# Kernel optimization log

Measured on AMD Instinct MI355X. Metric: run time of the kernel, lower is better.

The kernel has to match this reference:

```python
import jax, jax.numpy as jnp
import numpy as np

D = 1024
KERNEL = 4

def setup_inputs() -> dict:
    key = jax.random.key(0)
    ks = jax.random.split(key, 8)
    B, L, d = 4, 8192, D
    x = jax.random.normal(ks[0], (B, L, d), dtype=jnp.float32)
    conv_weight = jax.random.normal(ks[1], (d, 1, KERNEL), dtype=jnp.float32) * 0.02
    conv_bias = jnp.zeros((d,), dtype=jnp.float32)
    lim = 1.0 / np.sqrt(d)
    Wr_w = jax.random.uniform(ks[2], (d, d), jnp.float32, -lim, lim)
    Wr_b = jax.random.uniform(ks[3], (d,), jnp.float32, -lim, lim)
    Wi_w = jax.random.uniform(ks[4], (d, d), jnp.float32, -lim, lim)
    Wi_b = jax.random.uniform(ks[5], (d,), jnp.float32, -lim, lim)
    log_a = jnp.full((d,), 7.5, dtype=jnp.float32)
    out_w = jax.random.uniform(ks[6], (d, d), jnp.float32, -lim, lim)
    norm_w = jnp.ones((d,), dtype=jnp.float32)
    return {"x": x, "conv_weight": conv_weight, "conv_bias": conv_bias,
            "Wr_w": Wr_w, "Wr_b": Wr_b, "Wi_w": Wi_w, "Wi_b": Wi_b,
            "log_a": log_a, "out_w": out_w, "norm_w": norm_w}

def _causal_depthwise_conv(x, w, b):
    # x: [B,L,d], w: [d,1,K], b: [d]. out[t] = sum_k w[:,0,k] * x[t-3+k] + b
    B, L, d = x.shape
    xp = jnp.pad(x, ((0, 0), (KERNEL - 1, 0), (0, 0)))
    out = b[None, None, :]
    for k in range(KERNEL):  # small fixed kernel loop
        out = out + xp[:, k:k + L, :] * w[:, 0, k][None, None, :]
    return out

def _parallel_scan(a_t, b_t):
    # h_t = a_t * h_{t-1} + b_t via log-space cumsum; float32 throughout
    a = a_t.astype(jnp.float32)
    b = b_t.astype(jnp.float32)
    log_A = jnp.clip(jnp.cumsum(jnp.log(jnp.clip(a, 1e-7)), axis=1), -80.0, None)
    A = jnp.exp(log_A)
    h = A * jnp.cumsum(b * jnp.exp(-log_A), axis=1)
    return h.astype(a_t.dtype)

def _rmsnorm(x, w, eps=1e-6):
    ms = jnp.mean(jnp.square(x.astype(jnp.float32)), axis=-1, keepdims=True)
    return (x * jax.lax.rsqrt(ms + eps)).astype(x.dtype) * w

def reference(x, conv_weight, conv_bias, Wr_w, Wr_b, Wi_w, Wi_b, log_a, out_w, norm_w):
    x_conv = _causal_depthwise_conv(x, conv_weight, conv_bias)          # [B,L,d]
    r_t = jax.nn.sigmoid(x_conv @ Wr_w.T + Wr_b)
    i_t = jax.nn.sigmoid(x_conv @ Wi_w.T + Wi_b)
    a_base = jax.nn.sigmoid(log_a.astype(jnp.float32)).astype(x.dtype)
    a_t = jnp.power(a_base[None, None, :], 8.0 * r_t)
    b_t = jnp.sqrt(jnp.clip(1.0 - a_t * a_t, 1e-6, None)) * (i_t * x_conv)
    h = _parallel_scan(a_t, b_t)
    return _rmsnorm(h @ out_w.T, norm_w)
```

## Files before the change

kernel.cpp:

```cpp
#include <hip/hip_runtime.h>
#include <hip/hip_bf16.h>

#define D 1024
#define KW 4
#define SEQL 8192
#define BATCH 4
#define MROWS (BATCH*SEQL)
#define SEG 128
#define NSEG (SEQL/SEG)

using bf16 = __hip_bfloat16;
typedef __attribute__((ext_vector_type(8))) short bf16x8_t;
typedef __attribute__((ext_vector_type(4))) float f32x4_t;

__device__ __forceinline__ float sigmoid_f(float x){ return 1.0f/(1.0f + __expf(-x)); }

__device__ __forceinline__ void gload_lds16(const bf16* g, bf16* l){
  __builtin_amdgcn_global_load_lds(
    (const __attribute__((address_space(1))) unsigned int*)g,
    (__attribute__((address_space(3))) unsigned int*)l,
    16, 0, 0);
}

__device__ __forceinline__ void bf16x2_unpack(unsigned int u, float& lo, float& hi){
  union { unsigned int i; float f; } a, b;
  a.i = (u & 0xffffu) << 16;
  b.i = u & 0xffff0000u;
  lo = a.f; hi = b.f;
}
__device__ __forceinline__ unsigned int bf16x2_pack(float lo, float hi){
  unsigned short l = __builtin_bit_cast(unsigned short, __float2bfloat16(lo));
  unsigned short h = __builtin_bit_cast(unsigned short, __float2bfloat16(hi));
  return (unsigned int)l | ((unsigned int)h << 16);
}

__global__ __launch_bounds__(256) void prep_k(const float* __restrict__ Wr, const float* __restrict__ Wi,
                                              const float* __restrict__ Wrb, const float* __restrict__ Wib,
                                              const float* __restrict__ Wo,
                                              bf16* __restrict__ W1, bf16* __restrict__ Wob,
                                              float* __restrict__ b1){
  int idx = blockIdx.x*256 + threadIdx.x;
  if (idx < 2*D*D){
    int n = idx >> 10;
    float v = (n < D) ? Wr[idx] : Wi[idx - D*D];
    W1[idx] = __float2bfloat16(v);
  } else if (idx < 3*D*D){
    int j = idx - 2*D*D;
    Wob[j] = __float2bfloat16(Wo[j]);
  }
  if (idx < 2*D){
    b1[idx] = (idx < D) ? Wrb[idx] : Wib[idx - D];
  }
}

__global__ __launch_bounds__(256) void conv_k(const float* __restrict__ x, const float* __restrict__ w,
                                              const float* __restrict__ bias,
                                              unsigned int* __restrict__ xcb){
  int idx = blockIdx.x*256 + threadIdx.x;
  int c2 = idx & 511;
  int c  = c2 * 2;
  int m  = idx >> 9;
  int l  = m & (SEQL-1);
  const float* wp = w + c*KW;
  float2 b2 = *(const float2*)(bias + c);
  const float* xm = x + (size_t)m*D + c;
  float2 v3 = *(const float2*)xm;
  float2 v2 = (l>=1)? *(const float2*)(xm - D)   : make_float2(0.f,0.f);
  float2 v1 = (l>=2)? *(const float2*)(xm - 2*D) : make_float2(0.f,0.f);
  float2 v0 = (l>=3)? *(const float2*)(xm - 3*D) : make_float2(0.f,0.f);
  float a0 = b2.x + wp[0]*v0.x + wp[1]*v1.x + wp[2]*v2.x + wp[3]*v3.x;
  float a1 = b2.y + wp[4]*v0.y + wp[5]*v1.y + wp[6]*v2.y + wp[7]*v3.y;
  xcb[idx] = bf16x2_pack(a0, a1);
}

template<typename OutT> __device__ __forceinline__ void store_cvt(OutT* p, float v);
template<> __device__ __forceinline__ void store_cvt<float>(float* p, float v){ *p = v; }
template<> __device__ __forceinline__ void store_cvt<bf16>(bf16* p, float v){ *p = __float2bfloat16(v); }

template<typename OutT, bool HB>
__global__ __launch_bounds__(256) void gemm_bt(const bf16* __restrict__ A, const bf16* __restrict__ B,
                                               const float* __restrict__ bias, OutT* __restrict__ C,
                                               int M, int N, int K){
  __shared__ bf16 As[128][32];
  __shared__ bf16 Bs[128][32];
  const int t    = threadIdx.x;
  const int m0   = blockIdx.x * 128;
  const int n0   = blockIdx.y * 128;
  const int wave = t >> 6, lane = t & 63;
  const int wm   = (wave >> 1) * 64, wn = (wave & 1) * 64;
  const int lrow = lane & 15, quad = lane >> 4;

  f32x4_t acc[4][4];
  #pragma unroll
  for (int i=0;i<4;i++)
    #pragma unroll
    for (int j=0;j<4;j++) acc[i][j] = (f32x4_t){0.f,0.f,0.f,0.f};

  const int srow = lane >> 2;
  const int sk8  = (lane & 3) * 8;
  const bf16* Ag = A + (size_t)(m0 + wave*32 + srow)*K + sk8;
  const bf16* Bg = B + (size_t)(n0 + wave*32 + srow)*K + sk8;
  bf16* As0 = &As[wave*32     ][0];
  bf16* As1 = &As[wave*32 + 16][0];
  bf16* Bs0 = &Bs[wave*32     ][0];
  bf16* Bs1 = &Bs[wave*32 + 16][0];
  const size_t r16 = (size_t)16*K;

  for (int k0 = 0; k0 < K; k0 += 32){
    __syncthreads();
    gload_lds16(Ag + k0,       As0);
    gload_lds16(Ag + k0 + r16, As1);
    gload_lds16(Bg + k0,       Bs0);
    gload_lds16(Bg + k0 + r16, Bs1);
    __syncthreads();
    bf16x8_t af[4], bfr[4];
    #pragma unroll
    for (int i=0;i<4;i++) af[i]  = *(const bf16x8_t*)&As[wm + i*16 + lrow][quad*8];
    #pragma unroll
    for (int i=0;i<4;i++) bfr[i] = *(const bf16x8_t*)&Bs[wn + i*16 + lrow][quad*8];
    #pragma unroll
    for (int i=0;i<4;i++)
      #pragma unroll
      for (int j=0;j<4;j++)
        acc[i][j] = __builtin_amdgcn_mfma_f32_16x16x32_bf16(af[i], bfr[j], acc[i][j], 0, 0, 0);
  }

  #pragma unroll
  for (int i=0;i<4;i++){
    #pragma unroll
    for (int j=0;j<4;j++){
      int gm0 = m0 + wm + i*16 + quad*4;
      int gn  = n0 + wn + j*16 + lrow;
      float bv = HB ? bias[gn] : 0.f;
      #pragma unroll
      for (int r=0;r<4;r++){
        float v = acc[i][j][r] + bv;
        store_cvt(&C[(size_t)(gm0 + r)*N + gn], v);
      }
    }
  }
}

__global__ __launch_bounds__(256) void scan1_k(const unsigned int* __restrict__ ri,
                                               const unsigned int* __restrict__ xcb,
                                               const float* __restrict__ log_a,
                                               float* __restrict__ Aprod, float* __restrict__ Hend){
  int idx = blockIdx.x*256 + threadIdx.x;
  int c2 = idx & 511;
  int c  = c2*2;
  int bs = idx >> 9;
  int s  = bs & (NSEG-1);
  int b  = bs >> 6;
  size_t m0 = (size_t)b*SEQL + (size_t)s*SEG;
  float2 la = *(const float2*)(log_a + c);
  float c1x = -8.f * log1pf(__expf(-la.x));
  float c1y = -8.f * log1pf(__expf(-la.y));
  float Ax=1.f, Ay=1.f, hx=0.f, hy=0.f;
  for (int l=0; l<SEG; l++){
    size_t m = m0 + l;
    float zrx, zry, zix, ziy, xvx, xvy;
    bf16x2_unpack(ri[m*D + c2],        zrx, zry);
    bf16x2_unpack(ri[m*D + 512 + c2],  zix, ziy);
    bf16x2_unpack(xcb[m*512 + c2],     xvx, xvy);
    float ax = __expf(c1x * sigmoid_f(zrx));
    float ay = __expf(c1y * sigmoid_f(zry));
    float btx = sqrtf(fmaxf(1.f - ax*ax, 1e-6f)) * sigmoid_f(zix) * xvx;
    float bty = sqrtf(fmaxf(1.f - ay*ay, 1e-6f)) * sigmoid_f(ziy) * xvy;
    Ax *= ax; Ay *= ay;
    hx = fmaf(ax, hx, btx);
    hy = fmaf(ay, hy, bty);
  }
  *(float2*)(Aprod + 2*idx) = make_float2(Ax, Ay);
  *(float2*)(Hend  + 2*idx) = make_float2(hx, hy);
}

__global__ __launch_bounds__(256) void scan2_k(const float* __restrict__ Aprod, const float* __restrict__ Hend,
                                               float* __restrict__ carry){
  int idx = blockIdx.x*256 + threadIdx.x;
  int c = idx & (D-1);
  int b = idx >> 10;
  float h = 0.f;
  #pragma unroll 8
  for (int s=0; s<NSEG; s++){
    int j = ((b*NSEG + s) << 10) + c;
    carry[j] = h;
    h = fmaf(Aprod[j], h, Hend[j]);
  }
}

__global__ __launch_bounds__(256) void scan3_k(const unsigned int* __restrict__ ri,
                                               const unsigned int* __restrict__ xcb,
                                               const float* __restrict__ log_a, const float* __restrict__ carry,
                                               unsigned int* __restrict__ hbuf){
  int idx = blockIdx.x*256 + threadIdx.x;
  int c2 = idx & 511;
  int c  = c2*2;
  int bs = idx >> 9;
  int s  = bs & (NSEG-1);
  int b  = bs >> 6;
  size_t m0 = (size_t)b*SEQL + (size_t)s*SEG;
  float2 la = *(const float2*)(log_a + c);
  float c1x = -8.f * log1pf(__expf(-la.x));
  float c1y = -8.f * log1pf(__expf(-la.y));
  float2 h2 = *(const float2*)(carry + 2*idx);
  float hx = h2.x, hy = h2.y;
  for (int l=0; l<SEG; l++){
    size_t m = m0 + l;
    float zrx, zry, zix, ziy, xvx, xvy;
    bf16x2_unpack(ri[m*D + c2],       zrx, zry);
    bf16x2_unpack(ri[m*D + 512 + c2], zix, ziy);
    bf16x2_unpack(xcb[m*512 + c2],    xvx, xvy);
    float ax = __expf(c1x * sigmoid_f(zrx));
    float ay = __expf(c1y * sigmoid_f(zry));
    float btx = sqrtf(fmaxf(1.f - ax*ax, 1e-6f)) * sigmoid_f(zix) * xvx;
    float bty = sqrtf(fmaxf(1.f - ay*ay, 1e-6f)) * sigmoid_f(ziy) * xvy;
    hx = fmaf(ax, hx, btx);
    hy = fmaf(ay, hy, bty);
    hbuf[m*512 + c2] = bf16x2_pack(hx, hy);
  }
}

__global__ __launch_bounds__(256) void rms_k(float* __restrict__ y, const float* __restrict__ nw){
  int row = blockIdx.x;
  int t   = threadIdx.x;
  float* yr = y + (size_t)row*D;
  f32x4_t v = *(const f32x4_t*)(yr + t*4);
  float ss = v[0]*v[0] + v[1]*v[1] + v[2]*v[2] + v[3]*v[3];
  #pragma unroll
  for (int off=32; off>0; off>>=1) ss += __shfl_down(ss, off);
  __shared__ float red[4];
  if ((t & 63) == 0) red[t>>6] = ss;
  __syncthreads();
  float tot = red[0] + red[1] + red[2] + red[3];
  float scale = rsqrtf(tot * (1.f/D) + 1e-6f);
  f32x4_t w = *(const f32x4_t*)(nw + t*4);
  f32x4_t o;
  #pragma unroll
  for (int k=0;k<4;k++) o[k] = v[k]*scale*w[k];
  *(f32x4_t*)(yr + t*4) = o;
}

extern "C" void kernel_launch(void* const* d_in, const int* in_sizes, int n_in,
                              void* d_out, int out_size, void* d_ws, size_t ws_size,
                              hipStream_t stream) {
  const float* x     = (const float*)d_in[0];
  const float* convw = (const float*)d_in[1];
  const float* convb = (const float*)d_in[2];
  const float* Wr_w  = (const float*)d_in[3];
  const float* Wr_b  = (const float*)d_in[4];
  const float* Wi_w  = (const float*)d_in[5];
  const float* Wi_b  = (const float*)d_in[6];
  const float* log_a = (const float*)d_in[7];
  const float* out_w = (const float*)d_in[8];
  const float* norm_w= (const float*)d_in[9];

  char* ws = (char*)d_ws;
  size_t off = 0;
  auto alloc = [&](size_t bytes)->char*{ char* p = ws + off; off += (bytes + 255) & ~(size_t)255; return p; };

  bf16*  xcb   = (bf16*) alloc((size_t)MROWS*D*2);
  bf16*  ri    = (bf16*) alloc((size_t)MROWS*2*D*2);
  bf16*  hbuf  = (bf16*) alloc((size_t)MROWS*D*2);
  bf16*  W1    = (bf16*) alloc((size_t)2*D*D*2);
  bf16*  Wob   = (bf16*) alloc((size_t)D*D*2);
  float* b1    = (float*)alloc((size_t)2*D*4);
  float* Aprod = (float*)alloc((size_t)BATCH*NSEG*D*4);
  float* Hend  = (float*)alloc((size_t)BATCH*NSEG*D*4);
  float* carry = (float*)alloc((size_t)BATCH*NSEG*D*4);
  float* y     = (float*)d_out;

  prep_k<<<dim3((3*D*D + 255)/256), dim3(256), 0, stream>>>(Wr_w, Wi_w, Wr_b, Wi_b, out_w, W1, Wob, b1);
  conv_k<<<dim3(MROWS*(D/2)/256), dim3(256), 0, stream>>>(x, convw, convb, (unsigned int*)xcb);
  gemm_bt<bf16, true><<<dim3(MROWS/128, (2*D)/128), dim3(256), 0, stream>>>(xcb, W1, b1, ri, MROWS, 2*D, D);
  scan1_k<<<dim3(BATCH*NSEG*(D/2)/256), dim3(256), 0, stream>>>((const unsigned int*)ri, (const unsigned int*)xcb, log_a, Aprod, Hend);
  scan2_k<<<dim3(BATCH*D/256), dim3(256), 0, stream>>>(Aprod, Hend, carry);
  scan3_k<<<dim3(BATCH*NSEG*(D/2)/256), dim3(256), 0, stream>>>((const unsigned int*)ri, (const unsigned int*)xcb, log_a, carry, (unsigned int*)hbuf);
  gemm_bt<float, false><<<dim3(MROWS/128, D/128), dim3(256), 0, stream>>>(hbuf, Wob, nullptr, y, MROWS, D, D);
  rms_k<<<dim3(MROWS), dim3(256), 0, stream>>>(y, norm_w);
}
```

Baseline: 818.2 us.

## Replace GEMM with 256x256 double-buffered, swizzled-LDS pipelined MFMA kernel

Replaces the simple 128x128 single-buffered GEMM with a 256x256-tile, 512-thread kernel. It double-buffers K=64 tiles in LDS via global_load_lds, interleaves staging with MFMA phases using explicit vmcnt waits and barriers, and XOR-swizzles LDS columns to avoid bank conflicts. It also remaps block IDs for L2 locality and raises MFMA priority with setprio. The aim is to hide global-load latency and raise MFMA utilisation for both projection GEMMs, at the cost of 128KB LDS per block, lower occupancy and fragile hand-tuned waitcnt logic.

```diff
diff --git a/kernel.cpp b/kernel.cpp
--- a/kernel.cpp
+++ b/kernel.cpp
@@ -77,65 +77,126 @@
 template<> __device__ __forceinline__ void store_cvt<float>(float* p, float v){ *p = v; }
 template<> __device__ __forceinline__ void store_cvt<bf16>(bf16* p, float v){ *p = __float2bfloat16(v); }
 
+#define MFMA_BF16(a,b,c) __builtin_amdgcn_mfma_f32_16x16x32_bf16((a),(b),(c),0,0,0)
+
+#define GPHASE(buf, q, STAGE_STMT, WAIT_STMT) do{                         \
+    bf16x8_t a0 = rdA(buf, 2*(q),   0);                                   \
+    bf16x8_t a1 = rdA(buf, 2*(q),   1);                                   \
+    bf16x8_t a2 = rdA(buf, 2*(q)+1, 0);                                   \
+    bf16x8_t a3 = rdA(buf, 2*(q)+1, 1);                                   \
+    if ((q) == 0){                                                        \
+      b00 = rdB(buf,0,0); b01 = rdB(buf,0,1);                             \
+      b10 = rdB(buf,1,0); b11 = rdB(buf,1,1);                             \
+      b20 = rdB(buf,2,0); b21 = rdB(buf,2,1);                             \
+      b30 = rdB(buf,3,0); b31 = rdB(buf,3,1);                             \
+    }                                                                     \
+    STAGE_STMT;                                                           \
+    WAIT_STMT;                                                            \
+    __builtin_amdgcn_s_barrier();                                         \
+    asm volatile("s_waitcnt lgkmcnt(0)" ::: "memory");                    \
+    __builtin_amdgcn_s_setprio(1);                                        \
+    acc[2*(q)  ][0] = MFMA_BF16(a0, b00, acc[2*(q)  ][0]);                \
+    acc[2*(q)  ][0] = MFMA_BF16(a1, b01, acc[2*(q)  ][0]);                \
+    acc[2*(q)  ][1] = MFMA_BF16(a0, b10, acc[2*(q)  ][1]);                \
+    acc[2*(q)  ][1] = MFMA_BF16(a1, b11, acc[2*(q)  ][1]);                \
+    acc[2*(q)  ][2] = MFMA_BF16(a0, b20, acc[2*(q)  ][2]);                \
+    acc[2*(q)  ][2] = MFMA_BF16(a1, b21, acc[2*(q)  ][2]);                \
+    acc[2*(q)  ][3] = MFMA_BF16(a0, b30, acc[2*(q)  ][3]);                \
+    acc[2*(q)  ][3] = MFMA_BF16(a1, b31, acc[2*(q)  ][3]);                \
+    acc[2*(q)+1][0] = MFMA_BF16(a2, b00, acc[2*(q)+1][0]);                \
+    acc[2*(q)+1][0] = MFMA_BF16(a3, b01, acc[2*(q)+1][0]);                \
+    acc[2*(q)+1][1] = MFMA_BF16(a2, b10, acc[2*(q)+1][1]);                \
+    acc[2*(q)+1][1] = MFMA_BF16(a3, b11, acc[2*(q)+1][1]);                \
+    acc[2*(q)+1][2] = MFMA_BF16(a2, b20, acc[2*(q)+1][2]);                \
+    acc[2*(q)+1][2] = MFMA_BF16(a3, b21, acc[2*(q)+1][2]);                \
+    acc[2*(q)+1][3] = MFMA_BF16(a2, b30, acc[2*(q)+1][3]);                \
+    acc[2*(q)+1][3] = MFMA_BF16(a3, b31, acc[2*(q)+1][3]);                \
+    __builtin_amdgcn_s_setprio(0);                                        \
+    __builtin_amdgcn_s_barrier();                                         \
+}while(0)
+
+#define WAIT_STEADY do{ if (it + 1 < nIter) asm volatile("s_waitcnt vmcnt(4)" ::: "memory"); \
+                        else                asm volatile("s_waitcnt vmcnt(0)" ::: "memory"); }while(0)
+
 template<typename OutT, bool HB>
-__global__ __launch_bounds__(256) void gemm_bt(const bf16* __restrict__ A, const bf16* __restrict__ B,
-                                               const float* __restrict__ bias, OutT* __restrict__ C,
-                                               int M, int N, int K){
-  __shared__ bf16 As[128][32];
-  __shared__ bf16 Bs[128][32];
+__global__ __launch_bounds__(512, 2) void gemm256(const bf16* __restrict__ A, const bf16* __restrict__ B,
+                                                  const float* __restrict__ bias, OutT* __restrict__ C,
+                                                  int M, int N, int K){
+  __shared__ alignas(128) bf16 Asm[2][256*64];
+  __shared__ alignas(128) bf16 Bsm[2][256*64];
   const int t    = threadIdx.x;
-  const int m0   = blockIdx.x * 128;
-  const int n0   = blockIdx.y * 128;
   const int wave = t >> 6, lane = t & 63;
-  const int wm   = (wave >> 1) * 64, wn = (wave & 1) * 64;
+  const int wm   = wave >> 2, wn = wave & 3;
   const int lrow = lane & 15, quad = lane >> 4;
 
-  f32x4_t acc[4][4];
+  const int nbn = N >> 8;
+  const int cpx = gridDim.x >> 3;
+  const int bid = blockIdx.x;
+  const int swz = (bid & 7) * cpx + (bid >> 3);
+  const int m0  = (swz / nbn) << 8;
+  const int n0  = (swz % nbn) << 8;
+
+  const int srow = wave*8 + (lane >> 3);
+  const int scol = (((lane & 7) ^ (srow & 7)) << 3);
+
+  auto stageA = [&](int tile, int half, int buf){
+    const bf16* g = A + (size_t)(m0 + half*128 + srow)*K + tile*64 + scol;
+    bf16* l = &Asm[buf][half*128*64 + wave*8*64];
+    gload_lds16(g, l);
+    gload_lds16(g + (size_t)64*K, l + 64*64);
+  };
+  auto stageB = [&](int tile, int half, int buf){
+    const bf16* g = B + (size_t)(n0 + half*128 + srow)*K + tile*64 + scol;
+    bf16* l = &Bsm[buf][half*128*64 + wave*8*64];
+    gload_lds16(g, l);
+    gload_lds16(g + (size_t)64*K, l + 64*64);
+  };
+  auto rdA = [&](int buf, int fi, int ks)->bf16x8_t{
+    return *(const bf16x8_t*)&Asm[buf][(wm*128 + fi*16 + lrow)*64 + ((((ks)*4 + quad) ^ (lrow & 7)) << 3)];
+  };
+  auto rdB = [&](int buf, int j, int ks)->bf16x8_t{
+    return *(const bf16x8_t*)&Bsm[buf][(wn*64 + j*16 + lrow)*64 + ((((ks)*4 + quad) ^ (lrow & 7)) << 3)];
+  };
+
+  f32x4_t acc[8][4];
   #pragma unroll
-  for (int i=0;i<4;i++)
+  for (int i=0;i<8;i++)
     #pragma unroll
     for (int j=0;j<4;j++) acc[i][j] = (f32x4_t){0.f,0.f,0.f,0.f};
-
-  const int srow = lane >> 2;
-  const int sk8  = (lane & 3) * 8;
-  const bf16* Ag = A + (size_t)(m0 + wave*32 + srow)*K + sk8;
-  const bf16* Bg = B + (size_t)(n0 + wave*32 + srow)*K + sk8;
-  bf16* As0 = &As[wave*32     ][0];
-  bf16* As1 = &As[wave*32 + 16][0];
-  bf16* Bs0 = &Bs[wave*32     ][0];
-  bf16* Bs1 = &Bs[wave*32 + 16][0];
-  const size_t r16 = (size_t)16*K;
-
-  for (int k0 = 0; k0 < K; k0 += 32){
-    __syncthreads();
-    gload_lds16(Ag + k0,       As0);
-    gload_lds16(Ag + k0 + r16, As1);
-    gload_lds16(Bg + k0,       Bs0);
-    gload_lds16(Bg + k0 + r16, Bs1);
-    __syncthreads();
-    bf16x8_t af[4], bfr[4];
-    #pragma unroll
-    for (int i=0;i<4;i++) af[i]  = *(const bf16x8_t*)&As[wm + i*16 + lrow][quad*8];
-    #pragma unroll
-    for (int i=0;i<4;i++) bfr[i] = *(const bf16x8_t*)&Bs[wn + i*16 + lrow][quad*8];
-    #pragma unroll
-    for (int i=0;i<4;i++)
-      #pragma unroll
-      for (int j=0;j<4;j++)
-        acc[i][j] = __builtin_amdgcn_mfma_f32_16x16x32_bf16(af[i], bfr[j], acc[i][j], 0, 0, 0);
+  bf16x8_t b00,b01,b10,b11,b20,b21,b30,b31;
+
+  const int nt    = K >> 6;
+  const int nIter = nt >> 1;
+
+  stageB(0, 0, 0); stageB(0, 1, 0);
+  stageA(0, 0, 0); stageA(0, 1, 0);
+  stageB(1, 0, 1); stageB(1, 1, 1);
+  asm volatile("s_waitcnt vmcnt(4)" ::: "memory");
+  __builtin_amdgcn_s_barrier();
+
+  for (int it = 0; it < nIter; ++it){
+    const int t1 = 2*it + 1, t2 = 2*it + 2, t3 = 2*it + 3;
+    const bool ok2 = (t2 < nt), ok3 = (t3 < nt);
+    GPHASE(0, 0, stageA(t1, 0, 1), );
+    GPHASE(0, 1, stageA(t1, 1, 1), );
+    GPHASE(0, 2, if (ok2) stageB(t2, 0, 0), );
+    GPHASE(0, 3, if (ok2) stageB(t2, 1, 0), WAIT_STEADY);
+    GPHASE(1, 0, if (ok2) stageA(t2, 0, 0), );
+    GPHASE(1, 1, if (ok2) stageA(t2, 1, 0), );
+    GPHASE(1, 2, if (ok3) stageB(t3, 0, 1), );
+    GPHASE(1, 3, if (ok3) stageB(t3, 1, 1), WAIT_STEADY);
   }
 
   #pragma unroll
-  for (int i=0;i<4;i++){
+  for (int i=0;i<8;i++){
     #pragma unroll
     for (int j=0;j<4;j++){
-      int gm0 = m0 + wm + i*16 + quad*4;
-      int gn  = n0 + wn + j*16 + lrow;
+      int gm0 = m0 + wm*128 + i*16 + quad*4;
+      int gn  = n0 + wn*64  + j*16 + lrow;
       float bv = HB ? bias[gn] : 0.f;
       #pragma unroll
       for (int r=0;r<4;r++){
-        float v = acc[i][j][r] + bv;
-        store_cvt(&C[(size_t)(gm0 + r)*N + gn], v);
+        store_cvt(&C[(size_t)(gm0 + r)*N + gn], acc[i][j][r] + bv);
       }
     }
   }
@@ -271,10 +332,10 @@
 
   prep_k<<<dim3((3*D*D + 255)/256), dim3(256), 0, stream>>>(Wr_w, Wi_w, Wr_b, Wi_b, out_w, W1, Wob, b1);
   conv_k<<<dim3(MROWS*(D/2)/256), dim3(256), 0, stream>>>(x, convw, convb, (unsigned int*)xcb);
-  gemm_bt<bf16, true><<<dim3(MROWS/128, (2*D)/128), dim3(256), 0, stream>>>(xcb, W1, b1, ri, MROWS, 2*D, D);
+  gemm256<bf16, true><<<dim3((MROWS/256)*((2*D)/256)), dim3(512), 0, stream>>>(xcb, W1, b1, ri, MROWS, 2*D, D);
   scan1_k<<<dim3(BATCH*NSEG*(D/2)/256), dim3(256), 0, stream>>>((const unsigned int*)ri, (const unsigned int*)xcb, log_a, Aprod, Hend);
   scan2_k<<<dim3(BATCH*D/256), dim3(256), 0, stream>>>(Aprod, Hend, carry);
   scan3_k<<<dim3(BATCH*NSEG*(D/2)/256), dim3(256), 0, stream>>>((const unsigned int*)ri, (const unsigned int*)xcb, log_a, carry, (unsigned int*)hbuf);
-  gemm_bt<float, false><<<dim3(MROWS/128, D/128), dim3(256), 0, stream>>>(hbuf, Wob, nullptr, y, MROWS, D, D);
+  gemm256<float, false><<<dim3((MROWS/256)*(D/256)), dim3(512), 0, stream>>>(hbuf, Wob, nullptr, y, MROWS, D, D);
   rms_k<<<dim3(MROWS), dim3(256), 0, stream>>>(y, norm_w);
 }
```

New measurement: 740.6 us. 1.1x faster.
